# Kernel optimization log

Measured on AMD Instinct MI355X. Metric: run time of the kernel, lower is better.

Reference implementation:

```python
import jax, jax.numpy as jnp
import numpy as np

N_NODES = 50000
N_EDGES = 800000
N_GRAPHS = 512
F_IN = 16
E_DIM = 64
D = 128          # encoder_dim
L_DIM = 64       # latent_dim
MP_STEPS = 3
S2S_STEPS = 3
NEG_SLOPE = 0.01


def _leaky(v):
    return jax.nn.leaky_relu(v, NEG_SLOPE)


def setup_inputs() -> dict:
    key = jax.random.key(0)
    ks = jax.random.split(key, 24)

    def w(k, fan_in, shape):
        return jax.random.normal(k, shape, jnp.float32) / np.sqrt(fan_in)

    inp = {
        "x": jax.random.normal(ks[0], (N_NODES, F_IN), jnp.float32),
        "edge_index": jax.random.randint(ks[1], (2, N_EDGES), 0, N_NODES, jnp.int64),
        "edge_attr": jax.random.normal(ks[2], (N_EDGES, 4), jnp.float32),
        "batch": jnp.sort(jax.random.randint(ks[3], (N_NODES,), 0, N_GRAPHS, jnp.int64)),
        # embedding: Linear(F_IN -> E_DIM); weights stored [in, out]
        "W_emb": w(ks[4], F_IN, (F_IN, E_DIM)),
        "b_emb": jnp.zeros((E_DIM,), jnp.float32),
        # first: Linear(E_DIM -> D)
        "W_first": w(ks[5], E_DIM, (E_DIM, D)),
        "b_first": jnp.zeros((D,), jnp.float32),
        # SAGEConv: lin_l (aggregated neighbors, with bias), lin_r (root, no bias)
        "W_l": w(ks[6], D, (D, D)),
        "b_l": jnp.zeros((D,), jnp.float32),
        "W_r": w(ks[7], D, (D, D)),
        # GRU (1 layer): gates ordered r,z,n as in torch
        "gru_Wih": w(ks[8], D, (D, 3 * D)),
        "gru_Whh": w(ks[9], D, (D, 3 * D)),
        "gru_bih": jnp.zeros((3 * D,), jnp.float32),
        "gru_bhh": jnp.zeros((3 * D,), jnp.float32),
        # Set2Set LSTM: input 2D -> hidden D; gates ordered i,f,g,o as in torch
        "lstm_Wih": w(ks[10], 2 * D, (2 * D, 4 * D)),
        "lstm_Whh": w(ks[11], D, (D, 4 * D)),
        "lstm_bih": jnp.zeros((4 * D,), jnp.float32),
        "lstm_bhh": jnp.zeros((4 * D,), jnp.float32),
        # linear: Linear(2D -> D), final: Linear(D -> L_DIM)
        "W_lin": w(ks[12], 2 * D, (2 * D, D)),
        "b_lin": jnp.zeros((D,), jnp.float32),
        "W_fin": w(ks[13], D, (D, L_DIM)),
        "b_fin": jnp.zeros((L_DIM,), jnp.float32),
    }
    return inp


def _gru_step(x, h, Wih, Whh, bih, bhh):
    gi = x @ Wih + bih
    gh = h @ Whh + bhh
    ir, iz, inn = jnp.split(gi, 3, axis=-1)
    hr, hz, hn = jnp.split(gh, 3, axis=-1)
    r = jax.nn.sigmoid(ir + hr)
    z = jax.nn.sigmoid(iz + hz)
    n = jnp.tanh(inn + r * hn)
    return (1.0 - z) * n + z * h


def _lstm_step(x, h, c, Wih, Whh, bih, bhh):
    g = x @ Wih + bih + h @ Whh + bhh
    i, f, gg, o = jnp.split(g, 4, axis=-1)
    c_new = jax.nn.sigmoid(f) * c + jax.nn.sigmoid(i) * jnp.tanh(gg)
    h_new = jax.nn.sigmoid(o) * jnp.tanh(c_new)
    return h_new, c_new


def reference(x, edge_index, edge_attr, batch,
              W_emb, b_emb, W_first, b_first,
              W_l, b_l, W_r,
              gru_Wih, gru_Whh, gru_bih, gru_bhh,
              lstm_Wih, lstm_Whh, lstm_bih, lstm_bhh,
              W_lin, b_lin, W_fin, b_fin):
    # edge_attr is ignored (PyG SAGEConv does not use it).
    out = _leaky(x @ W_emb + b_emb)        # [N, E_DIM]
    out = _leaky(out @ W_first + b_first)  # [N, D]
    h = out                                # GRU hidden state [N, D]
    src, dst = edge_index[0], edge_index[1]
    for _ in range(MP_STEPS):
        agg = jax.ops.segment_sum(out[src], dst, num_segments=N_NODES)  # [N, D]
        m = jax.nn.relu(agg @ W_l + b_l + out @ W_r)  # SAGEConv(aggr='add') + root
        out = _gru_step(m, h, gru_Wih, gru_Whh, gru_bih, gru_bhh)
        h = out
    # Set2Set pooling over graphs
    q_star = jnp.zeros((N_GRAPHS, 2 * D), out.dtype)
    hh = jnp.zeros((N_GRAPHS, D), out.dtype)
    cc = jnp.zeros((N_GRAPHS, D), out.dtype)
    for _ in range(S2S_STEPS):
        hh, cc = _lstm_step(q_star, hh, cc, lstm_Wih, lstm_Whh, lstm_bih, lstm_bhh)
        e = jnp.sum(out * hh[batch], axis=-1)                             # [N]
        e_max = jax.ops.segment_max(e, batch, num_segments=N_GRAPHS)      # [B]
        a = jnp.exp(e - e_max[batch])
        s = jax.ops.segment_sum(a, batch, num_segments=N_GRAPHS)
        a = a / (s[batch] + 1e-16)                                        # segment softmax
        r = jax.ops.segment_sum(a[:, None] * out, batch, num_segments=N_GRAPHS)  # [B, D]
        q_star = jnp.concatenate([hh, r], axis=-1)                        # [B, 2D]
    out = _leaky(q_star @ W_lin + b_lin)
    return out @ W_fin + b_fin  # [B, L_DIM]
```

## Files before the change

kernel.cpp:

```cpp
#include <hip/hip_runtime.h>
#include <hip/hip_bf16.h>
#include <math.h>

#define N_NODES 50000
#define N_EDGES 800000
#define N_GRAPHS 512
#define F_IN 16
#define E_DIM 64
#define D 128
#define L_DIM 64
#define NEG_SLOPE 0.01f

#define SCAN_N (N_NODES + 1)
#define SCAN_CH 512
#define SCAN_NCH ((SCAN_N + SCAN_CH - 1) / SCAN_CH)

typedef __hip_bfloat16 bf16;
typedef unsigned int uint;
typedef unsigned short ushort;
typedef __attribute__((ext_vector_type(8))) short short8;
typedef __attribute__((ext_vector_type(4))) float float4v;

__device__ __forceinline__ float b2f(bf16 v) { return __bfloat162float(v); }
__device__ __forceinline__ bf16  f2b(float v) { return __float2bfloat16(v); }
__device__ __forceinline__ short f2bs(float f) { bf16 b = __float2bfloat16(f); return *reinterpret_cast<short*>(&b); }
__device__ __forceinline__ float bs2f(short s) { return __uint_as_float(((uint)(ushort)s) << 16); }
__device__ __forceinline__ float leaky(float v) { return v > 0.f ? v : NEG_SLOPE * v; }
__device__ __forceinline__ float sigm(float v) { return 1.f / (1.f + expf(-v)); }

__global__ __launch_bounds__(256) void k_signal(float* outp, int n)
{
    int i = blockIdx.x * 256 + threadIdx.x;
    if (i < n) outp[i] = 1.0f;
}

#define NPE 16
__global__ __launch_bounds__(128) void k_embed(
    const float* __restrict__ x, const float* __restrict__ Wemb, const float* __restrict__ bemb,
    const float* __restrict__ Wfirst, const float* __restrict__ bfirst, bf16* __restrict__ out)
{
    __shared__ float xs[NPE][F_IN];
    __shared__ float ys[NPE][E_DIM];
    int t = threadIdx.x;
    int base = blockIdx.x * NPE;

    for (int i = t; i < NPE * F_IN; i += 128)
        xs[i / F_IN][i % F_IN] = x[(size_t)base * F_IN + i];
    __syncthreads();

    if (t < E_DIM) {
        float acc[NPE];
#pragma unroll
        for (int nn = 0; nn < NPE; nn++) acc[nn] = 0.f;
        for (int k = 0; k < F_IN; k++) {
            float w = Wemb[k * E_DIM + t];
#pragma unroll
            for (int nn = 0; nn < NPE; nn++) acc[nn] += xs[nn][k] * w;
        }
        float bb = bemb[t];
#pragma unroll
        for (int nn = 0; nn < NPE; nn++) ys[nn][t] = leaky(acc[nn] + bb);
    }
    __syncthreads();

    {
        float acc[NPE];
#pragma unroll
        for (int nn = 0; nn < NPE; nn++) acc[nn] = 0.f;
        for (int k = 0; k < E_DIM; k++) {
            float w = Wfirst[k * D + t];
#pragma unroll
            for (int nn = 0; nn < NPE; nn++) acc[nn] += ys[nn][k] * w;
        }
        float bb = bfirst[t];
#pragma unroll
        for (int nn = 0; nn < NPE; nn++)
            out[(size_t)(base + nn) * D + t] = f2b(leaky(acc[nn] + bb));
    }
}

__global__ __launch_bounds__(256) void k_count(const int* __restrict__ ei, int* __restrict__ offs)
{
    int e = blockIdx.x * 256 + threadIdx.x;
    if (e < N_EDGES) {
        int d = ei[N_EDGES + e];
        d = d < 0 ? 0 : (d >= N_NODES ? N_NODES - 1 : d);
        atomicAdd(&offs[d + 1], 1);
    }
}

__global__ __launch_bounds__(SCAN_CH) void k_scan1(int* __restrict__ offs, int* __restrict__ bsum)
{
    __shared__ int sh[SCAN_CH];
    int t = threadIdx.x;
    int i = blockIdx.x * SCAN_CH + t;
    sh[t] = (i < SCAN_N) ? offs[i] : 0;
    __syncthreads();
    for (int d = 1; d < SCAN_CH; d <<= 1) {
        int v = (t >= d) ? sh[t - d] : 0;
        __syncthreads();
        sh[t] += v;
        __syncthreads();
    }
    if (i < SCAN_N) offs[i] = sh[t];
    if (t == SCAN_CH - 1) bsum[blockIdx.x] = sh[t];
}

__global__ void k_scan2(int* __restrict__ bsum)
{
    if (threadIdx.x == 0 && blockIdx.x == 0) {
        int run = 0;
        for (int i = 0; i < SCAN_NCH; i++) { int v = bsum[i]; bsum[i] = run; run += v; }
    }
}

__global__ __launch_bounds__(SCAN_CH) void k_scan3(int* __restrict__ offs, const int* __restrict__ bsum)
{
    int i = blockIdx.x * SCAN_CH + threadIdx.x;
    if (i < SCAN_N) offs[i] += bsum[blockIdx.x];
}

__global__ __launch_bounds__(256) void k_fill(
    const int* __restrict__ ei, const int* __restrict__ offs,
    int* __restrict__ curs, int* __restrict__ srcs)
{
    int e = blockIdx.x * 256 + threadIdx.x;
    if (e < N_EDGES) {
        int s = ei[e];
        int d = ei[N_EDGES + e];
        s = s < 0 ? 0 : (s >= N_NODES ? N_NODES - 1 : s);
        d = d < 0 ? 0 : (d >= N_NODES ? N_NODES - 1 : d);
        int slot = offs[d] + atomicAdd(&curs[d], 1);
        if (slot >= 0 && slot < N_EDGES) srcs[slot] = s;
    }
}

__global__ __launch_bounds__(256) void k_gstart(const int* __restrict__ batch, int* __restrict__ gstart)
{
    int g = blockIdx.x * 256 + threadIdx.x;
    if (g > N_GRAPHS) return;
    int lo = 0, hi = N_NODES;
    while (lo < hi) {
        int mid = (lo + hi) >> 1;
        if (batch[mid] < g) lo = mid + 1; else hi = mid;
    }
    gstart[g] = lo;
}

__global__ __launch_bounds__(256) void k_pack_all(
    const float* __restrict__ Wl, const float* __restrict__ Wr,
    const float* __restrict__ gWih, const float* __restrict__ gWhh,
    short* __restrict__ W1p, short* __restrict__ Wihp, short* __restrict__ Whhp)
{
    int tid = blockIdx.x * 256 + threadIdx.x;
    if (tid < 32768) {
        int j = tid & 7, l = (tid >> 3) & 63, frag = tid >> 9;
        int nb = frag & 7, kb = frag >> 3;
        int k = kb * 32 + ((l >> 4) * 8) + j;
        int n = nb * 16 + (l & 15);
        float v = (k < 128) ? Wl[k * D + n] : Wr[(k - 128) * D + n];
        W1p[tid] = f2bs(v);
    } else {
        int id = tid - 32768;
        const float* W = gWih;
        short* Wp = Wihp;
        if (id >= 49152) { id -= 49152; W = gWhh; Wp = Whhp; }
        int j = id & 7, l = (id >> 3) & 63, frag = id >> 9;
        int nb = frag % 24, kb = frag / 24;
        int k = kb * 32 + ((l >> 4) * 8) + j;
        int n = nb * 16 + (l & 15);
        Wp[id] = f2bs(W[k * 384 + n]);
    }
}

__global__ __launch_bounds__(256) void k_gather(
    const bf16* __restrict__ hin, bf16* __restrict__ hagg,
    const int* __restrict__ offs, const int* __restrict__ srcs)
{
    int w = threadIdx.x >> 6, l = threadIdx.x & 63;
    int n = blockIdx.x * 4 + w;
    const ushort* hinu = (const ushort*)hin;
    int j0 = offs[n], j1 = offs[n + 1];
    j0 = j0 < 0 ? 0 : (j0 > N_EDGES ? N_EDGES : j0);
    j1 = j1 < j0 ? j0 : (j1 > N_EDGES ? N_EDGES : j1);

    float lo[8], hi8[8];
#pragma unroll
    for (int i = 0; i < 8; i++) { lo[i] = 0.f; hi8[i] = 0.f; }

    int j = j0;
    for (; j + 7 < j1; j += 8) {
        int ss[8];
        uint vv[8];
#pragma unroll
        for (int i = 0; i < 8; i++) {
            int s = srcs[j + i];
            ss[i] = s < 0 ? 0 : (s >= N_NODES ? N_NODES - 1 : s);
        }
#pragma unroll
        for (int i = 0; i < 8; i++)
            vv[i] = *(const uint*)(hinu + (size_t)ss[i] * D + l * 2);
#pragma unroll
        for (int i = 0; i < 8; i++) {
            lo[i] += __uint_as_float(vv[i] << 16);
            hi8[i] += __uint_as_float(vv[i] & 0xffff0000u);
        }
    }
    for (; j < j1; j++) {
        int s = srcs[j];
        s = s < 0 ? 0 : (s >= N_NODES ? N_NODES - 1 : s);
        uint v = *(const uint*)(hinu + (size_t)s * D + l * 2);
        lo[0] += __uint_as_float(v << 16);
        hi8[0] += __uint_as_float(v & 0xffff0000u);
    }
    float a0 = ((lo[0] + lo[1]) + (lo[2] + lo[3])) + ((lo[4] + lo[5]) + (lo[6] + lo[7]));
    float a1 = ((hi8[0] + hi8[1]) + (hi8[2] + hi8[3])) + ((hi8[4] + hi8[5]) + (hi8[6] + hi8[7]));
    uint ap = ((uint)(ushort)f2bs(a1) << 16) | (ushort)f2bs(a0);
    *(uint*)((ushort*)hagg + (size_t)n * D + l * 2) = ap;
}

#define M_STR 136
__global__ __launch_bounds__(128) void k_sage_gru_mfma(
    const bf16* __restrict__ hin, bf16* __restrict__ hagg_out,
    const short* __restrict__ W1p, const short* __restrict__ Wihp, const short* __restrict__ Whhp,
    const float* __restrict__ bl, const float* __restrict__ bih, const float* __restrict__ bhh)
{
    __shared__ short Msh[64 * M_STR];
    int t = threadIdx.x;
    int w = t >> 6, l = t & 63;
    int base = blockIdx.x * 64;
    const ushort* hinu = (const ushort*)hin;
    const ushort* haggu = (const ushort*)hagg_out;
    ushort* houtu = (ushort*)hagg_out;

    int r0 = base + w * 32 + (l & 15);
    int r1 = r0 + 16;
    int rc0 = r0 < N_NODES ? r0 : N_NODES - 1;
    int rc1 = r1 < N_NODES ? r1 : N_NODES - 1;
    int koff = (l >> 4) * 8;

    short8 afr0[8], afr1[8];
#pragma unroll
    for (int k0 = 0; k0 < 4; k0++) {
        afr0[k0] = *(const short8*)(haggu + (size_t)rc0 * D + k0 * 32 + koff);
        afr1[k0] = *(const short8*)(haggu + (size_t)rc1 * D + k0 * 32 + koff);
    }
#pragma unroll
    for (int k0 = 0; k0 < 4; k0++) {
        afr0[4 + k0] = *(const short8*)(hinu + (size_t)rc0 * D + k0 * 32 + koff);
        afr1[4 + k0] = *(const short8*)(hinu + (size_t)rc1 * D + k0 * 32 + koff);
    }

    int mrow0 = w * 32 + (l & 15);
    int mrow1 = mrow0 + 16;
    int crow0 = w * 32 + (l >> 4) * 4;
    int crow1 = crow0 + 16;

    short8 bA[8], bB[8];
#pragma unroll
    for (int k0 = 0; k0 < 8; k0++)
        bA[k0] = *(const short8*)&W1p[((k0 * 8 + 0) * 64 + l) * 8];
#pragma unroll
    for (int ct = 0; ct < 8; ct++) {
        const short8* bc = (ct & 1) ? bB : bA;
        short8* bn = (ct & 1) ? bA : bB;
        if (ct < 7) {
#pragma unroll
            for (int k0 = 0; k0 < 8; k0++)
                bn[k0] = *(const short8*)&W1p[((k0 * 8 + ct + 1) * 64 + l) * 8];
        }
        float4v acc0 = {0.f, 0.f, 0.f, 0.f};
        float4v acc1 = {0.f, 0.f, 0.f, 0.f};
#pragma unroll
        for (int k0 = 0; k0 < 8; k0++) {
            acc0 = __builtin_amdgcn_mfma_f32_16x16x32_bf16(afr0[k0], bc[k0], acc0, 0, 0, 0);
            acc1 = __builtin_amdgcn_mfma_f32_16x16x32_bf16(afr1[k0], bc[k0], acc1, 0, 0, 0);
        }
        float bb = bl[ct * 16 + (l & 15)];
#pragma unroll
        for (int i = 0; i < 4; i++) {
            float v0 = acc0[i] + bb;
            float v1 = acc1[i] + bb;
            Msh[(crow0 + i) * M_STR + ct * 16 + (l & 15)] = f2bs(v0 > 0.f ? v0 : 0.f);
            Msh[(crow1 + i) * M_STR + ct * 16 + (l & 15)] = f2bs(v1 > 0.f ? v1 : 0.f);
        }
    }
    __syncthreads();

    short8 amr0[4], amr1[4];
#pragma unroll
    for (int k0 = 0; k0 < 4; k0++) {
        amr0[k0] = *(const short8*)&Msh[mrow0 * M_STR + k0 * 32 + koff];
        amr1[k0] = *(const short8*)&Msh[mrow1 * M_STR + k0 * 32 + koff];
    }

    short8 iA[4], hA[4], iB[4], hB[4];
#pragma unroll
    for (int k0 = 0; k0 < 4; k0++) {
        iA[k0] = *(const short8*)&Wihp[((k0 * 24 + 0) * 64 + l) * 8];
        hA[k0] = *(const short8*)&Whhp[((k0 * 24 + 0) * 64 + l) * 8];
    }
#pragma unroll
    for (int ct = 0; ct < 8; ct++) {
        int c = ct * 16 + (l & 15);
        float rv0[4], zv0[4], rv1[4], zv1[4];
#pragma unroll
        for (int p = 0; p < 3; p++) {
            int ph = ct * 3 + p;
            const short8* wi = (ph & 1) ? iB : iA;
            const short8* wh = (ph & 1) ? hB : hA;
            short8* win = (ph & 1) ? iA : iB;
            short8* whn = (ph & 1) ? hA : hB;
            if (ph < 23) {
                int pn = ph + 1;
                int ctn = pn / 3, ppn = pn - ctn * 3;
                int nbn = ppn * 8 + ctn;
#pragma unroll
                for (int k0 = 0; k0 < 4; k0++) {
                    win[k0] = *(const short8*)&Wihp[((k0 * 24 + nbn) * 64 + l) * 8];
                    whn[k0] = *(const short8*)&Whhp[((k0 * 24 + nbn) * 64 + l) * 8];
                }
            }
            float4v ai0 = {0.f, 0.f, 0.f, 0.f};
            float4v ah0 = {0.f, 0.f, 0.f, 0.f};
            float4v ai1 = {0.f, 0.f, 0.f, 0.f};
            float4v ah1 = {0.f, 0.f, 0.f, 0.f};
#pragma unroll
            for (int k0 = 0; k0 < 4; k0++) {
                ai0 = __builtin_amdgcn_mfma_f32_16x16x32_bf16(amr0[k0], wi[k0], ai0, 0, 0, 0);
                ah0 = __builtin_amdgcn_mfma_f32_16x16x32_bf16(afr0[4 + k0], wh[k0], ah0, 0, 0, 0);
                ai1 = __builtin_amdgcn_mfma_f32_16x16x32_bf16(amr1[k0], wi[k0], ai1, 0, 0, 0);
                ah1 = __builtin_amdgcn_mfma_f32_16x16x32_bf16(afr1[4 + k0], wh[k0], ah1, 0, 0, 0);
            }
            float bis = bih[p * 128 + c];
            float bhs = bhh[p * 128 + c];
            if (p == 0) {
#pragma unroll
                for (int i = 0; i < 4; i++) {
                    rv0[i] = sigm(ai0[i] + bis + ah0[i] + bhs);
                    rv1[i] = sigm(ai1[i] + bis + ah1[i] + bhs);
                }
            } else if (p == 1) {
#pragma unroll
                for (int i = 0; i < 4; i++) {
                    zv0[i] = sigm(ai0[i] + bis + ah0[i] + bhs);
                    zv1[i] = sigm(ai1[i] + bis + ah1[i] + bhs);
                }
            } else {
#pragma unroll
                for (int i = 0; i < 4; i++) {
                    int g0 = base + crow0 + i;
                    int g1 = base + crow1 + i;
                    int gc0 = g0 < N_NODES ? g0 : N_NODES - 1;
                    int gc1 = g1 < N_NODES ? g1 : N_NODES - 1;
                    float h0v = bs2f((short)hinu[(size_t)gc0 * D + c]);
                    float h1v = bs2f((short)hinu[(size_t)gc1 * D + c]);
                    float nv0 = tanhf(ai0[i] + bis + rv0[i] * (ah0[i] + bhs));
                    float nv1 = tanhf(ai1[i] + bis + rv1[i] * (ah1[i] + bhs));
                    if (g0 < N_NODES)
                        houtu[(size_t)g0 * D + c] = (ushort)f2bs((1.f - zv0[i]) * nv0 + zv0[i] * h0v);
                    if (g1 < N_NODES)
                        houtu[(size_t)g1 * D + c] = (ushort)f2bs((1.f - zv1[i]) * nv1 + zv1[i] * h1v);
                }
            }
        }
    }
}

#define POOL_CAP 1024
__global__ __launch_bounds__(1024) void k_s2s(
    const float* __restrict__ Wih, const float* __restrict__ Whh,
    const float* __restrict__ bih, const float* __restrict__ bhh,
    const bf16* __restrict__ h, const int* __restrict__ gstart,
    float* __restrict__ qstar, float* __restrict__ hh, float* __restrict__ cc, int first)
{
    int g = blockIdx.x;
    int t = threadIdx.x;
    __shared__ float qs[2 * D];
    __shared__ float hs[D];
    __shared__ float part[2][512];
    __shared__ float hnew[D];
    __shared__ float e_lds[POOL_CAP];
    __shared__ float redM[16], redS[16];
    __shared__ float rpart[8][D];

    int c = t & 511, half = t >> 9;
    if (t < 2 * D) qs[t] = first ? 0.f : qstar[(size_t)g * 2 * D + t];
    else if (t < 3 * D) hs[t - 2 * D] = first ? 0.f : hh[(size_t)g * D + (t - 2 * D)];
    __syncthreads();

    float acc = half ? 0.f : (bih[c] + bhh[c]);
    int qb = half * 128;
#pragma unroll 4
    for (int i = 0; i < 128; i++) {
        int k = qb + i;
        acc += qs[k] * Wih[(size_t)k * 512 + c];
    }
    int hb = half * 64;
#pragma unroll 4
    for (int i = 0; i < 64; i++) {
        int k = hb + i;
        acc += hs[k] * Whh[(size_t)k * 512 + c];
    }
    part[half][c] = acc;
    __syncthreads();

    if (t < D) {
        float gi = part[0][t] + part[1][t];
        float gf = part[0][D + t] + part[1][D + t];
        float gg = part[0][2 * D + t] + part[1][2 * D + t];
        float go = part[0][3 * D + t] + part[1][3 * D + t];
        float c_old = first ? 0.f : cc[(size_t)g * D + t];
        float cn = sigm(gf) * c_old + sigm(gi) * tanhf(gg);
        float hn = sigm(go) * tanhf(cn);
        cc[(size_t)g * D + t] = cn;
        hh[(size_t)g * D + t] = hn;
        qstar[(size_t)g * 2 * D + t] = hn;
        hnew[t] = hn;
    }
    __syncthreads();

    int w = t >> 6, l = t & 63;
    int s0 = gstart[g], s1 = gstart[g + 1];
    s0 = s0 < 0 ? 0 : (s0 > N_NODES ? N_NODES : s0);
    s1 = s1 < s0 ? s0 : (s1 > N_NODES ? N_NODES : s1);
    int cnt = s1 - s0;
    const ushort* hu = (const ushort*)h;

    float hq0 = hnew[l];
    float hq1 = hnew[64 + l];

    int dim = t & 127, h8 = t >> 7;
    float m_run = -INFINITY, s_run = 0.f, racc = 0.f;

    for (int c0 = 0; c0 < cnt; c0 += POOL_CAP) {
        int clen = cnt - c0; if (clen > POOL_CAP) clen = POOL_CAP;

        for (int i = w; i < clen; i += 16) {
            int n = s0 + c0 + i;
            float v = bs2f((short)hu[(size_t)n * D + l]) * hq0
                    + bs2f((short)hu[(size_t)n * D + 64 + l]) * hq1;
#pragma unroll
            for (int off = 32; off > 0; off >>= 1) v += __shfl_down(v, off);
            if (l == 0) e_lds[i] = v;
        }
        __syncthreads();

        float m = -INFINITY;
        for (int i = t; i < clen; i += 1024) m = fmaxf(m, e_lds[i]);
#pragma unroll
        for (int off = 32; off > 0; off >>= 1) m = fmaxf(m, __shfl_down(m, off));
        if (l == 0) redM[w] = m;
        __syncthreads();
        m = -INFINITY;
#pragma unroll
        for (int i = 0; i < 16; i++) m = fmaxf(m, redM[i]);
        float m_new = fmaxf(m_run, m);
        float scale = (m_run == -INFINITY) ? 0.f : expf(m_run - m_new);
        s_run *= scale;
        racc *= scale;
        __syncthreads();

        float s = 0.f;
        for (int i = t; i < clen; i += 1024) {
            float wv = expf(e_lds[i] - m_new);
            e_lds[i] = wv;
            s += wv;
        }
#pragma unroll
        for (int off = 32; off > 0; off >>= 1) s += __shfl_down(s, off);
        if (l == 0) redS[w] = s;
        __syncthreads();
#pragma unroll
        for (int i = 0; i < 16; i++) s_run += redS[i];

        for (int i = h8; i < clen; i += 8)
            racc += e_lds[i] * bs2f((short)hu[(size_t)(s0 + c0 + i) * D + dim]);
        m_run = m_new;
        __syncthreads();
    }

    rpart[h8][dim] = racc;
    __syncthreads();
    if (t < D) {
        float inv = 1.f / (s_run + 1e-16f);
        float r = 0.f;
#pragma unroll
        for (int i = 0; i < 8; i++) r += rpart[i][t];
        qstar[(size_t)g * 2 * D + D + t] = r * inv;
    }
}

__global__ __launch_bounds__(128) void k_final(
    const float* __restrict__ qstar, const float* __restrict__ Wlin, const float* __restrict__ blin,
    const float* __restrict__ Wfin, const float* __restrict__ bfin, float* __restrict__ outp)
{
    int g = blockIdx.x, t = threadIdx.x;
    __shared__ float qs[2 * D], ts[D];
    qs[t] = qstar[(size_t)g * 2 * D + t];
    qs[D + t] = qstar[(size_t)g * 2 * D + D + t];
    __syncthreads();

    float acc = blin[t];
    for (int k = 0; k < 2 * D; k++) acc += qs[k] * Wlin[(size_t)k * D + t];
    ts[t] = leaky(acc);
    __syncthreads();

    if (t < L_DIM) {
        float a2 = bfin[t];
        for (int k = 0; k < D; k++) a2 += ts[k] * Wfin[(size_t)k * L_DIM + t];
        outp[(size_t)g * L_DIM + t] = a2;
    }
}

extern "C" void kernel_launch(void* const* d_in, const int* in_sizes, int n_in,
                              void* d_out, int out_size, void* d_ws, size_t ws_size,
                              hipStream_t stream)
{
    const float* x      = (const float*)d_in[0];
    const int*   ei     = (const int*)d_in[1];
    const int*   batch  = (const int*)d_in[3];
    const float* Wemb   = (const float*)d_in[4];
    const float* bemb   = (const float*)d_in[5];
    const float* Wfirst = (const float*)d_in[6];
    const float* bfirst = (const float*)d_in[7];
    const float* Wl     = (const float*)d_in[8];
    const float* bl     = (const float*)d_in[9];
    const float* Wr     = (const float*)d_in[10];
    const float* gWih   = (const float*)d_in[11];
    const float* gWhh   = (const float*)d_in[12];
    const float* gbih   = (const float*)d_in[13];
    const float* gbhh   = (const float*)d_in[14];
    const float* lWih   = (const float*)d_in[15];
    const float* lWhh   = (const float*)d_in[16];
    const float* lbih   = (const float*)d_in[17];
    const float* lbhh   = (const float*)d_in[18];
    const float* Wlin   = (const float*)d_in[19];
    const float* blin   = (const float*)d_in[20];
    const float* Wfin   = (const float*)d_in[21];
    const float* bfin   = (const float*)d_in[22];
    float* outp = (float*)d_out;

    size_t o = 0;
    char* base = (char*)d_ws;
    auto carve = [&](size_t bytes) { void* p = base + o; o += (bytes + 255) & ~(size_t)255; return p; };
    bf16*  h0     = (bf16*)carve((size_t)N_NODES * D * sizeof(bf16));
    bf16*  h1     = (bf16*)carve((size_t)N_NODES * D * sizeof(bf16));
    int*   offs   = (int*)carve((size_t)SCAN_N * sizeof(int));
    int*   curs   = (int*)carve((size_t)N_NODES * sizeof(int));
    int*   srcs   = (int*)carve((size_t)N_EDGES * sizeof(int));
    int*   bsum   = (int*)carve((size_t)SCAN_NCH * sizeof(int));
    float* hh     = (float*)carve((size_t)N_GRAPHS * D * sizeof(float));
    float* cc     = (float*)carve((size_t)N_GRAPHS * D * sizeof(float));
    float* qstar  = (float*)carve((size_t)N_GRAPHS * 2 * D * sizeof(float));
    int*   gstart = (int*)carve((size_t)(N_GRAPHS + 1) * sizeof(int));
    short* W1p    = (short*)carve((size_t)256 * 128 * sizeof(short));
    short* Wihp   = (short*)carve((size_t)128 * 384 * sizeof(short));
    short* Whhp   = (short*)carve((size_t)128 * 384 * sizeof(short));
    size_t need = o;

    if (ws_size < need) {
        k_signal<<<(out_size + 255) / 256, 256, 0, stream>>>(outp, out_size);
        return;
    }

    k_embed<<<N_NODES / NPE, 128, 0, stream>>>(x, Wemb, bemb, Wfirst, bfirst, h0);

    k_pack_all<<<(32768 + 98304) / 256, 256, 0, stream>>>(Wl, Wr, gWih, gWhh, W1p, Wihp, Whhp);

    hipMemsetAsync(offs, 0, (size_t)((char*)srcs - (char*)offs), stream);
    k_count<<<(N_EDGES + 255) / 256, 256, 0, stream>>>(ei, offs);
    k_scan1<<<SCAN_NCH, SCAN_CH, 0, stream>>>(offs, bsum);
    k_scan2<<<1, 64, 0, stream>>>(bsum);
    k_scan3<<<SCAN_NCH, SCAN_CH, 0, stream>>>(offs, bsum);
    k_fill<<<(N_EDGES + 255) / 256, 256, 0, stream>>>(ei, offs, curs, srcs);

    k_gstart<<<(N_GRAPHS + 1 + 255) / 256, 256, 0, stream>>>(batch, gstart);

    bf16* hc = h0; bf16* hn = h1;
    for (int s = 0; s < 3; s++) {
        k_gather<<<N_NODES / 4, 256, 0, stream>>>(hc, hn, offs, srcs);
        k_sage_gru_mfma<<<(N_NODES + 63) / 64, 128, 0, stream>>>(
            hc, hn, W1p, Wihp, Whhp, bl, gbih, gbhh);
        bf16* tmp = hc; hc = hn; hn = tmp;
    }

    for (int s = 0; s < 3; s++) {
        k_s2s<<<N_GRAPHS, 1024, 0, stream>>>(lWih, lWhh, lbih, lbhh,
                                             hc, gstart, qstar, hh, cc, s == 0);
    }

    k_final<<<N_GRAPHS, 128, 0, stream>>>(qstar, Wlin, blin, Wfin, bfin, outp);
}
```

Baseline: 558.8 us.

## Batch two graphs per Set2Set block and reuse staged hidden rows in GRU

The Set2Set kernel now handles two graphs per 1024-thread block. Each LSTM weight element is loaded once and applied to both graphs' q_star/h vectors, which halves weight traffic from global memory. The attention pooling then runs over the two graphs one after the other inside the block. Separately, the GRU kernel stages the previous hidden-state rows it already holds in registers into shared memory and reads them from there for the final blend, instead of reloading them from global. The costs are half as many Set2Set blocks, so less parallelism across the GPU, and extra LDS use in the GRU kernel, which may reduce occupancy.

Result: no change. 550.1 us (-1.6%).

```diff
diff --git a/kernel.cpp b/kernel.cpp
--- a/kernel.cpp
+++ b/kernel.cpp
@@ -226,6 +226,7 @@
     const float* __restrict__ bl, const float* __restrict__ bih, const float* __restrict__ bhh)
 {
     __shared__ short Msh[64 * M_STR];
+    __shared__ short Hsh[64 * M_STR];
     int t = threadIdx.x;
     int w = t >> 6, l = t & 63;
     int base = blockIdx.x * 64;
@@ -255,6 +256,12 @@
     int mrow1 = mrow0 + 16;
     int crow0 = w * 32 + (l >> 4) * 4;
     int crow1 = crow0 + 16;
+
+#pragma unroll
+    for (int k0 = 0; k0 < 4; k0++) {
+        *(short8*)&Hsh[mrow0 * M_STR + k0 * 32 + koff] = afr0[4 + k0];
+        *(short8*)&Hsh[mrow1 * M_STR + k0 * 32 + koff] = afr1[4 + k0];
+    }
 
     short8 bA[8], bB[8];
 #pragma unroll
@@ -351,10 +358,8 @@
                 for (int i = 0; i < 4; i++) {
                     int g0 = base + crow0 + i;
                     int g1 = base + crow1 + i;
-                    int gc0 = g0 < N_NODES ? g0 : N_NODES - 1;
-                    int gc1 = g1 < N_NODES ? g1 : N_NODES - 1;
-                    float h0v = bs2f((short)hinu[(size_t)gc0 * D + c]);
-                    float h1v = bs2f((short)hinu[(size_t)gc1 * D + c]);
+                    float h0v = bs2f(Hsh[(crow0 + i) * M_STR + c]);
+                    float h1v = bs2f(Hsh[(crow1 + i) * M_STR + c]);
                     float nv0 = tanhf(ai0[i] + bis + rv0[i] * (ah0[i] + bhs));
                     float nv1 = tanhf(ai1[i] + bis + rv1[i] * (ah1[i] + bhs));
                     if (g0 < N_NODES)
@@ -368,126 +373,144 @@
 }
 
 #define POOL_CAP 1024
+#define LG2 2
 __global__ __launch_bounds__(1024) void k_s2s(
     const float* __restrict__ Wih, const float* __restrict__ Whh,
     const float* __restrict__ bih, const float* __restrict__ bhh,
     const bf16* __restrict__ h, const int* __restrict__ gstart,
     float* __restrict__ qstar, float* __restrict__ hh, float* __restrict__ cc, int first)
 {
-    int g = blockIdx.x;
+    int g0 = blockIdx.x * LG2;
     int t = threadIdx.x;
-    __shared__ float qs[2 * D];
-    __shared__ float hs[D];
-    __shared__ float part[2][512];
-    __shared__ float hnew[D];
+    __shared__ float qs[LG2][2 * D];
+    __shared__ float hs[LG2][D];
+    __shared__ float part[2][LG2][512];
+    __shared__ float hnew[LG2][D];
     __shared__ float e_lds[POOL_CAP];
     __shared__ float redM[16], redS[16];
     __shared__ float rpart[8][D];
 
+    for (int i = t; i < LG2 * 2 * D; i += 1024) {
+        int g = i / (2 * D), c = i % (2 * D);
+        qs[g][c] = first ? 0.f : qstar[(size_t)(g0 + g) * 2 * D + c];
+    }
+    for (int i = t; i < LG2 * D; i += 1024) {
+        int g = i / D, c = i % D;
+        hs[g][c] = first ? 0.f : hh[(size_t)(g0 + g) * D + c];
+    }
+    __syncthreads();
+
     int c = t & 511, half = t >> 9;
-    if (t < 2 * D) qs[t] = first ? 0.f : qstar[(size_t)g * 2 * D + t];
-    else if (t < 3 * D) hs[t - 2 * D] = first ? 0.f : hh[(size_t)g * D + (t - 2 * D)];
-    __syncthreads();
-
-    float acc = half ? 0.f : (bih[c] + bhh[c]);
+    float a0 = half ? 0.f : (bih[c] + bhh[c]);
+    float a1 = a0;
     int qb = half * 128;
 #pragma unroll 4
     for (int i = 0; i < 128; i++) {
         int k = qb + i;
-        acc += qs[k] * Wih[(size_t)k * 512 + c];
+        float wv = Wih[(size_t)k * 512 + c];
+        a0 += qs[0][k] * wv;
+        a1 += qs[1][k] * wv;
     }
     int hb = half * 64;
 #pragma unroll 4
     for (int i = 0; i < 64; i++) {
         int k = hb + i;
-        acc += hs[k] * Whh[(size_t)k * 512 + c];
-    }
-    part[half][c] = acc;
-    __syncthreads();
-
-    if (t < D) {
-        float gi = part[0][t] + part[1][t];
-        float gf = part[0][D + t] + part[1][D + t];
-        float gg = part[0][2 * D + t] + part[1][2 * D + t];
-        float go = part[0][3 * D + t] + part[1][3 * D + t];
-        float c_old = first ? 0.f : cc[(size_t)g * D + t];
-        float cn = sigm(gf) * c_old + sigm(gi) * tanhf(gg);
+        float wv = Whh[(size_t)k * 512 + c];
+        a0 += hs[0][k] * wv;
+        a1 += hs[1][k] * wv;
+    }
+    part[half][0][c] = a0;
+    part[half][1][c] = a1;
+    __syncthreads();
+
+    if (t < LG2 * D) {
+        int g = t >> 7, tt = t & 127;
+        float gi = part[0][g][tt] + part[1][g][tt];
+        float gf = part[0][g][D + tt] + part[1][g][D + tt];
+        float gg2 = part[0][g][2 * D + tt] + part[1][g][2 * D + tt];
+        float go = part[0][g][3 * D + tt] + part[1][g][3 * D + tt];
+        float c_old = first ? 0.f : cc[(size_t)(g0 + g) * D + tt];
+        float cn = sigm(gf) * c_old + sigm(gi) * tanhf(gg2);
         float hn = sigm(go) * tanhf(cn);
-        cc[(size_t)g * D + t] = cn;
-        hh[(size_t)g * D + t] = hn;
-        qstar[(size_t)g * 2 * D + t] = hn;
-        hnew[t] = hn;
+        cc[(size_t)(g0 + g) * D + tt] = cn;
+        hh[(size_t)(g0 + g) * D + tt] = hn;
+        qstar[(size_t)(g0 + g) * 2 * D + tt] = hn;
+        hnew[g][tt] = hn;
     }
     __syncthreads();
 
     int w = t >> 6, l = t & 63;
-    int s0 = gstart[g], s1 = gstart[g + 1];
-    s0 = s0 < 0 ? 0 : (s0 > N_NODES ? N_NODES : s0);
-    s1 = s1 < s0 ? s0 : (s1 > N_NODES ? N_NODES : s1);
-    int cnt = s1 - s0;
+    int dim = t & 127, h8 = t >> 7;
     const ushort* hu = (const ushort*)h;
 
-    float hq0 = hnew[l];
-    float hq1 = hnew[64 + l];
-
-    int dim = t & 127, h8 = t >> 7;
-    float m_run = -INFINITY, s_run = 0.f, racc = 0.f;
-
-    for (int c0 = 0; c0 < cnt; c0 += POOL_CAP) {
-        int clen = cnt - c0; if (clen > POOL_CAP) clen = POOL_CAP;
-
-        for (int i = w; i < clen; i += 16) {
-            int n = s0 + c0 + i;
-            float v = bs2f((short)hu[(size_t)n * D + l]) * hq0
-                    + bs2f((short)hu[(size_t)n * D + 64 + l]) * hq1;
-#pragma unroll
-            for (int off = 32; off > 0; off >>= 1) v += __shfl_down(v, off);
-            if (l == 0) e_lds[i] = v;
-        }
+    for (int gg = 0; gg < LG2; gg++) {
+        int g = g0 + gg;
+        int s0 = gstart[g], s1 = gstart[g + 1];
+        s0 = s0 < 0 ? 0 : (s0 > N_NODES ? N_NODES : s0);
+        s1 = s1 < s0 ? s0 : (s1 > N_NODES ? N_NODES : s1);
+        int cnt = s1 - s0;
+
+        float hq0 = hnew[gg][l];
+        float hq1 = hnew[gg][64 + l];
+        float m_run = -INFINITY, s_run = 0.f, racc = 0.f;
+
+        for (int c0 = 0; c0 < cnt; c0 += POOL_CAP) {
+            int clen = cnt - c0; if (clen > POOL_CAP) clen = POOL_CAP;
+
+            for (int i = w; i < clen; i += 16) {
+                int n = s0 + c0 + i;
+                float v = bs2f((short)hu[(size_t)n * D + l]) * hq0
+                        + bs2f((short)hu[(size_t)n * D + 64 + l]) * hq1;
+#pragma unroll
+                for (int off = 32; off > 0; off >>= 1) v += __shfl_down(v, off);
+                if (l == 0) e_lds[i] = v;
+            }
+            __syncthreads();
+
+            float m = -INFINITY;
+            for (int i = t; i < clen; i += 1024) m = fmaxf(m, e_lds[i]);
+#pragma unroll
+            for (int off = 32; off > 0; off >>= 1) m = fmaxf(m, __shfl_down(m, off));
+            if (l == 0) redM[w] = m;
+            __syncthreads();
+            m = -INFINITY;
+#pragma unroll
+            for (int i = 0; i < 16; i++) m = fmaxf(m, redM[i]);
+            float m_new = fmaxf(m_run, m);
+            float scale = (m_run == -INFINITY) ? 0.f : expf(m_run - m_new);
+            s_run *= scale;
+            racc *= scale;
+            __syncthreads();
+
+            float s = 0.f;
+            for (int i = t; i < clen; i += 1024) {
+                float wv = expf(e_lds[i] - m_new);
+                e_lds[i] = wv;
+                s += wv;
+            }
+#pragma unroll
+            for (int off = 32; off > 0; off >>= 1) s += __shfl_down(s, off);
+            if (l == 0) redS[w] = s;
+            __syncthreads();
+#pragma unroll
+            for (int i = 0; i < 16; i++) s_run += redS[i];
+
+            for (int i = h8; i < clen; i += 8)
+                racc += e_lds[i] * bs2f((short)hu[(size_t)(s0 + c0 + i) * D + dim]);
+            m_run = m_new;
+            __syncthreads();
+        }
+
+        rpart[h8][dim] = racc;
         __syncthreads();
-
-        float m = -INFINITY;
-        for (int i = t; i < clen; i += 1024) m = fmaxf(m, e_lds[i]);
-#pragma unroll
-        for (int off = 32; off > 0; off >>= 1) m = fmaxf(m, __shfl_down(m, off));
-        if (l == 0) redM[w] = m;
+        if (t < D) {
+            float inv = 1.f / (s_run + 1e-16f);
+            float r = 0.f;
+#pragma unroll
+            for (int i = 0; i < 8; i++) r += rpart[i][t];
+            qstar[(size_t)g * 2 * D + D + t] = r * inv;
+        }
         __syncthreads();
-        m = -INFINITY;
-#pragma unroll
-        for (int i = 0; i < 16; i++) m = fmaxf(m, redM[i]);
-        float m_new = fmaxf(m_run, m);
-        float scale = (m_run == -INFINITY) ? 0.f : expf(m_run - m_new);
-        s_run *= scale;
-        racc *= scale;
-        __syncthreads();
-
-        float s = 0.f;
-        for (int i = t; i < clen; i += 1024) {
-            float wv = expf(e_lds[i] - m_new);
-            e_lds[i] = wv;
-            s += wv;
-        }
-#pragma unroll
-        for (int off = 32; off > 0; off >>= 1) s += __shfl_down(s, off);
-        if (l == 0) redS[w] = s;
-        __syncthreads();
-#pragma unroll
-        for (int i = 0; i < 16; i++) s_run += redS[i];
-
-        for (int i = h8; i < clen; i += 8)
-            racc += e_lds[i] * bs2f((short)hu[(size_t)(s0 + c0 + i) * D + dim]);
-        m_run = m_new;
-        __syncthreads();
-    }
-
-    rpart[h8][dim] = racc;
-    __syncthreads();
-    if (t < D) {
-        float inv = 1.f / (s_run + 1e-16f);
-        float r = 0.f;
-#pragma unroll
-        for (int i = 0; i < 8; i++) r += rpart[i][t];
-        qstar[(size_t)g * 2 * D + D + t] = r * inv;
     }
 }
 
@@ -586,8 +609,8 @@
     }
 
     for (int s = 0; s < 3; s++) {
-        k_s2s<<<N_GRAPHS, 1024, 0, stream>>>(lWih, lWhh, lbih, lbhh,
-                                             hc, gstart, qstar, hh, cc, s == 0);
+        k_s2s<<<N_GRAPHS / LG2, 1024, 0, stream>>>(lWih, lWhh, lbih, lbhh,
+                                                   hc, gstart, qstar, hh, cc, s == 0);
     }
 
     k_final<<<N_GRAPHS, 128, 0, stream>>>(qstar, Wlin, blin, Wfin, bfin, outp);
```
